# Optimization experiments

Measured on AMD Instinct MI355X. Metric: run time of the kernel, lower is better.

Reference implementation:

```python
import jax, jax.numpy as jnp
import numpy as np

# Dims (see shape_source)
B, C_IN, H, W = 32, 256, 56, 56
O, J = 256, 64            # out_channels, in_connects (sparse in-channel subset per out channel)
KH, KW = 3, 3
STRIDE = (1, 1)
PAD = (1, 1)


def setup_inputs() -> dict:
    key = jax.random.key(0)
    k1, k2 = jax.random.split(key)
    x = jax.random.normal(k1, (B, C_IN, H, W), dtype=jnp.float32)
    # init_rand_indices: each out channel samples in_connects distinct in-channels
    rng = np.random.default_rng(0)
    w_idx = jnp.asarray(
        np.stack([rng.permutation(C_IN)[:J] for _ in range(O)]), dtype=jnp.int32
    )  # [O, J]
    # reset_parameters: uniform(-stdv, +stdv), stdv = 1/sqrt(in_connects * kh * kw)
    stdv = 1.0 / np.sqrt(J * KH * KW)
    w_vals = jax.random.uniform(k2, (O, J, KH, KW), dtype=jnp.float32,
                                minval=-stdv, maxval=stdv)
    return {"x": x, "w_vals": w_vals, "w_idx": w_idx}


def reference(x, w_vals, w_idx):
    # Sparse conv: out[b,o] = sum_j conv(x[:, w_idx[o,j]], w_vals[o,j]).
    # Equivalent math: scatter sparse weights into a dense [O, C_in, KH, KW]
    # kernel (zeros on unselected channels) and run one dense conv.
    dense_w = jnp.zeros((O, C_IN, KH, KW), dtype=w_vals.dtype)
    dense_w = dense_w.at[jnp.arange(O)[:, None], w_idx].set(w_vals)
    out = jax.lax.conv_general_dilated(
        x, dense_w,
        window_strides=STRIDE,
        padding=[(PAD[0], PAD[0]), (PAD[1], PAD[1])],
        dimension_numbers=("NCHW", "OIHW", "NCHW"),
    )  # [B, O, H, W]
    return out
```

## Files before the change

### kernel.cpp

```cpp
#include <hip/hip_runtime.h>
#include <hip/hip_bf16.h>


typedef __attribute__((ext_vector_type(8))) short bf16x8;
typedef __attribute__((ext_vector_type(4))) float f32x4;

#define WD_BYTES 1179648
#define XP_BYTES 55115776
#define WS_NEED  (WD_BYTES + XP_BYTES)
#define ABUF  32768
#define BHOFF 65536
#define LDS_TOT (65536 + 49152)

__global__ __launch_bounds__(256) void preproc(
    const float* __restrict__ x, const float* __restrict__ wv,
    const int* __restrict__ widx, __hip_bfloat16* __restrict__ wd,
    __hip_bfloat16* __restrict__ xp)
{
    int bid = blockIdx.x;
    int tid = threadIdx.x;
    if (bid >= 1792) {
        int o = bid - 1792;
        int j = tid & 63;
        if (tid < 64) {
#pragma unroll
            for (int k = 0; k < 9; ++k)
                reinterpret_cast<float2*>(wd + (size_t)k * 65536 + o * 256)[j] =
                    float2{0.f, 0.f};
        }
        __syncthreads();
        if (tid < 64) {
            int cin = widx[o * 64 + j];
            const float* src = wv + (size_t)(o * 64 + j) * 9;
#pragma unroll
            for (int k = 0; k < 9; ++k)
                wd[(size_t)k * 65536 + o * 256 + cin] = __float2bfloat16(src[k]);
        }
        return;
    }
    int b = bid / 56, h = bid - (bid / 56) * 56;
    __shared__ __hip_bfloat16 tile[56][264];
    int c = tid;
    const float* src = x + ((size_t)(b * 256 + c)) * 3136 + h * 56;
    float vals[56];
#pragma unroll
    for (int i = 0; i < 14; ++i) {
        float4 v = *reinterpret_cast<const float4*>(src + i * 4);
        vals[i*4+0] = v.x; vals[i*4+1] = v.y; vals[i*4+2] = v.z; vals[i*4+3] = v.w;
    }
#pragma unroll
    for (int w = 0; w < 56; ++w) tile[w][c] = __float2bfloat16(vals[w]);

    char* rowb = (char*)xp + (((size_t)b * 58 + (h + 1)) * 58) * 512;
    if (tid < 64)        reinterpret_cast<double*>(rowb)[tid] = 0.0;
    else if (tid < 128)  *reinterpret_cast<double*>(rowb + 57 * 512 + (tid - 64) * 8) = 0.0;
    if (h == 0) {
        char* r0 = (char*)xp + (((size_t)b * 58 + 0) * 58) * 512;
        for (int i = tid; i < 58 * 64; i += 256) reinterpret_cast<double*>(r0)[i] = 0.0;
    }
    if (h == 55) {
        char* r57 = (char*)xp + (((size_t)b * 58 + 57) * 58) * 512;
        for (int i = tid; i < 58 * 64; i += 256) reinterpret_cast<double*>(r57)[i] = 0.0;
    }

    __syncthreads();
    char* obase = (char*)xp + (((size_t)b * 58 + (h + 1)) * 58) * 512;
#pragma unroll
    for (int k = 0; k < 7; ++k) {
        int i = tid + k * 256;
        int w = i >> 5, cc = i & 31;
        bf16x8 v = *reinterpret_cast<const bf16x8*>(&tile[w][cc * 8]);
        *reinterpret_cast<bf16x8*>(obase + (size_t)(w + 1) * 512 + cc * 16) = v;
    }
}


__device__ __forceinline__ void gload_lds16(const void* g, void* l) {
    __builtin_amdgcn_global_load_lds(
        (const __attribute__((address_space(1))) void*)g,
        (__attribute__((address_space(3))) void*)l, 16, 0, 0);
}

__device__ __forceinline__ void stage_a4(const char* wdB, char* smem, int dstA,
                                         int wid, int sa_off, int aoff) {
#pragma unroll
    for (int J = 0; J < 4; ++J)
        gload_lds16(wdB + aoff + J * 32768 + sa_off,
                    smem + dstA + (J * 64 + wid * 8) * 128);
}

__device__ __forceinline__ void stage_bh6(const char* xpOcs, char* smem, int wid,
                                          const int (&srcp)[6]) {
#pragma unroll
    for (int j = 0; j < 6; ++j)
        gload_lds16(xpOcs + srcp[j], smem + BHOFF + j * 8192 + wid * 1024);
}

#define BAR() __builtin_amdgcn_s_barrier()
#define VMCNT0() asm volatile("s_waitcnt vmcnt(0)" ::: "memory")

__global__ __launch_bounds__(512, 2) void sparse_conv_mfma224(
    const __hip_bfloat16* __restrict__ wd, const __hip_bfloat16* __restrict__ xp,
    float* __restrict__ out)
{
    extern __shared__ char smem[];
    const char* wdB = (const char*)wd;
    const char* xpB = (const char*)xp;

    const int bid = blockIdx.x;
    const int nt = (bid & 7) * 56 + (bid >> 3);

    const int t = threadIdx.x;
    const int lane = t & 63, wid = t >> 6;
    const int wr = wid >> 1, wc = wid & 1;

    const int axor = (((lane & 7) ^ (lane >> 3)) * 16);
    const int sa_off = (wid * 8 + (lane >> 3)) * 512 + axor;

    const int a_rb = (lane & 15) * 128;
    const int xq0 = (((lane >> 4)) ^ (lane & 7)) * 16;
    const int xq1 = ((4 + (lane >> 4)) ^ (lane & 7)) * 16;
    const int wrOff = wr * 8192;

    const int p0 = nt * 224;
    const int bImg = p0 / 3136;
    const int r0 = (p0 - bImg * 3136) / 56;
    const char* xpO = xpB + (size_t)((bImg * 58 + r0) * 58) * 512;

    int srcp[6];
#pragma unroll
    for (int j = 0; j < 6; ++j) {
        int beta = j * 8192 + wid * 1024 + lane * 16;
        int rb = beta >> 7;
        int c  = (beta >> 4) & 7;
        srcp[j] = (rb < 348) ? (rb * 512 + ((c ^ (rb & 7)) << 4)) : 0;
    }

    int rowpl[7];
#pragma unroll
    for (int n = 0; n < 7; ++n) {
        int q = wc * 112 + n * 16 + (lane & 15);
        int qr = q / 56;
        rowpl[n] = qr * 58 + (q - qr * 56);
    }
    const int g4 = lane >> 4;

    f32x4 acc[4][7] = {};

    stage_bh6(xpO, smem, wid, srcp);
    stage_a4(wdB, smem, 0, wid, sa_off, 0);
    VMCNT0();
    BAR();

    int k9 = 0, cs = 0, shift = 0;
    for (int g = 0; g < 36; ++g) {
        int k9n = k9 + 1, csn = cs;
        if (k9n == 9) { k9n = 0; csn = cs + 1; if (csn == 4) csn = 0; }
        stage_a4(wdB, smem, ((g + 1) & 1) * ABUF, wid, sa_off,
                 k9n * 131072 + csn * 128);

        const int abase = (g & 1) * ABUF + wrOff + a_rb;
        bf16x8 af0[4], af1[4], bf0[7], bf1[7];
#pragma unroll
        for (int mi = 0; mi < 4; ++mi) {
            af0[mi] = *(const bf16x8*)(smem + abase + mi * 2048 + xq0);
            af1[mi] = *(const bf16x8*)(smem + abase + mi * 2048 + xq1);
        }
#pragma unroll
        for (int n = 0; n < 7; ++n) {
            int roff = rowpl[n] + shift;
            int ba = BHOFF + (roff << 7) + ((g4 ^ (roff & 7)) << 4);
            bf0[n] = *(const bf16x8*)(smem + ba);
            bf1[n] = *(const bf16x8*)(smem + (ba ^ 64));
        }

        __builtin_amdgcn_s_setprio(1);
#pragma unroll
        for (int mi = 0; mi < 4; ++mi)
#pragma unroll
            for (int ni = 0; ni < 7; ++ni)
                acc[mi][ni] = __builtin_amdgcn_mfma_f32_16x16x32_bf16(
                    af0[mi], bf0[ni], acc[mi][ni], 0, 0, 0);
#pragma unroll
        for (int mi = 0; mi < 4; ++mi)
#pragma unroll
            for (int ni = 0; ni < 7; ++ni)
                acc[mi][ni] = __builtin_amdgcn_mfma_f32_16x16x32_bf16(
                    af1[mi], bf1[ni], acc[mi][ni], 0, 0, 0);
        __builtin_amdgcn_s_setprio(0);

        VMCNT0();
        BAR();

        if (k9n == 0) {
            if (csn != 0) {
                stage_bh6(xpO + csn * 128, smem, wid, srcp);
                VMCNT0();
                BAR();
            }
            shift = 0;
        } else {
            shift += ((k9n % 3) == 0) ? 56 : 1;
        }
        k9 = k9n; cs = csn;
    }

#pragma unroll
    for (int n = 0; n < 7; ++n) {
        int p = nt * 224 + wc * 112 + n * 16;
        int pb = p / 3136;
        int rem0 = p - pb * 3136;
#pragma unroll
        for (int m = 0; m < 4; ++m) {
            int o = wr * 64 + m * 16 + (lane >> 4) * 4;
            float* dst = out + ((size_t)(pb * 256 + o)) * 3136 + rem0 + (lane & 15);
#pragma unroll
            for (int r = 0; r < 4; ++r) dst[(size_t)r * 3136] = acc[m][n][r];
        }
    }
}


__global__ __launch_bounds__(256) void sparse_conv_direct(
    const float* __restrict__ x, const float* __restrict__ wv,
    const int* __restrict__ widx, float* __restrict__ out)
{
    const int bid = blockIdx.x;
    const int b = bid >> 8, o = bid & 255;
    const int tid = threadIdx.x;
    __shared__ float plane[58 * 60];
    const int rt = tid >> 3, ct = tid & 7;
    const int r0 = rt * 2, c0 = ct * 7;
    const bool active = (rt < 28);
    float acc[2][7];
#pragma unroll
    for (int i = 0; i < 2; ++i)
#pragma unroll
        for (int c = 0; c < 7; ++c) acc[i][c] = 0.f;
    const float* xb = x + (size_t)b * 256 * 3136;
    const int* idxp = widx + o * 64;
    const float* wp0 = wv + (size_t)o * 64 * 9;
    for (int j = 0; j < 64; ++j) {
        const int cin = idxp[j];
        const float* src = xb + cin * 3136;
        __syncthreads();
        for (int i = tid; i < 58 * 58; i += 256) {
            const int r = i / 58, c = i - r * 58;
            const int h = r - 1, w = c - 1;
            float v = 0.f;
            if ((unsigned)h < 56u && (unsigned)w < 56u) v = src[h * 56 + w];
            plane[r * 60 + c] = v;
        }
        float wreg[9];
#pragma unroll
        for (int k = 0; k < 9; ++k) wreg[k] = wp0[j * 9 + k];
        __syncthreads();
        if (active) {
            float rows[4][9];
#pragma unroll
            for (int dr = 0; dr < 4; ++dr)
#pragma unroll
                for (int cc = 0; cc < 9; ++cc)
                    rows[dr][cc] = plane[(r0 + dr) * 60 + (c0 + cc)];
#pragma unroll
            for (int i = 0; i < 2; ++i)
#pragma unroll
                for (int cc = 0; cc < 7; ++cc) {
                    float s = acc[i][cc];
#pragma unroll
                    for (int kh = 0; kh < 3; ++kh)
#pragma unroll
                        for (int kw = 0; kw < 3; ++kw)
                            s += rows[i + kh][cc + kw] * wreg[kh * 3 + kw];
                    acc[i][cc] = s;
                }
        }
    }
    if (active) {
        float* op = out + (size_t)bid * 3136;
#pragma unroll
        for (int i = 0; i < 2; ++i)
#pragma unroll
            for (int cc = 0; cc < 7; ++cc)
                op[(r0 + i) * 56 + (c0 + cc)] = acc[i][cc];
    }
}

extern "C" void kernel_launch(void* const* d_in, const int* in_sizes, int n_in,
                              void* d_out, int out_size, void* d_ws, size_t ws_size,
                              hipStream_t stream) {
    const float* x    = (const float*)d_in[0];
    const float* wv   = (const float*)d_in[1];
    const int*   widx = (const int*)d_in[2];
    float* out = (float*)d_out;
    (void)in_sizes; (void)n_in; (void)out_size;

    if (ws_size < (size_t)WS_NEED) {
        sparse_conv_direct<<<dim3(32 * 256), dim3(256), 0, stream>>>(x, wv, widx, out);
        return;
    }

    __hip_bfloat16* wd = (__hip_bfloat16*)d_ws;
    __hip_bfloat16* xp = (__hip_bfloat16*)((char*)d_ws + WD_BYTES);

    preproc<<<dim3(32 * 56 + 256), dim3(256), 0, stream>>>(x, wv, widx, wd, xp);

    (void)hipFuncSetAttribute((const void*)sparse_conv_mfma224,
                              hipFuncAttributeMaxDynamicSharedMemorySize, LDS_TOT);
    sparse_conv_mfma224<<<dim3(448), dim3(512), LDS_TOT, stream>>>(wd, xp, out);
}
```

Baseline: 150.0 us.

## Triple-buffer weight tiles and split K-halves to overlap LDS reads with MFMA

```diff
diff --git a/kernel.cpp b/kernel.cpp
--- a/kernel.cpp
+++ b/kernel.cpp
@@ -9,8 +9,8 @@
 #define XP_BYTES 55115776
 #define WS_NEED  (WD_BYTES + XP_BYTES)
 #define ABUF  32768
-#define BHOFF 65536
-#define LDS_TOT (65536 + 49152)
+#define BHOFF 98304
+#define LDS_TOT 147456
 
 __global__ __launch_bounds__(256) void preproc(
     const float* __restrict__ x, const float* __restrict__ wv,
@@ -99,6 +99,67 @@
 #define BAR() __builtin_amdgcn_s_barrier()
 #define VMCNT0() asm volatile("s_waitcnt vmcnt(0)" ::: "memory")
 
+__device__ __forceinline__ void mfma28(bf16x8 (&af)[4], bf16x8 (&bf)[7],
+                                       f32x4 (&acc)[4][7]) {
+    __builtin_amdgcn_s_setprio(1);
+#pragma unroll
+    for (int mi = 0; mi < 4; ++mi)
+#pragma unroll
+        for (int ni = 0; ni < 7; ++ni)
+            acc[mi][ni] = __builtin_amdgcn_mfma_f32_16x16x32_bf16(
+                af[mi], bf[ni], acc[mi][ni], 0, 0, 0);
+    __builtin_amdgcn_s_setprio(0);
+}
+
+template<int TJ>
+__device__ __forceinline__ void iter_normal(
+    const char* wdB, char* smem, int cs,
+    int wid, int sa_off, int wrOff, int a_rb, int xq0, int xq1, int g4,
+    const int (&rowpl)[7], bf16x8 (&bf0)[7], f32x4 (&acc)[4][7])
+{
+    constexpr int E   = TJ % 3;
+    constexpr int E2  = (TJ + 2) % 3;
+    constexpr int SH  = (TJ / 3) * 58 + (TJ % 3);
+    constexpr int SHN = ((TJ + 1) / 3) * 58 + ((TJ + 1) % 3);
+
+    bf16x8 af1[4], bf1[7];
+    {
+        const int abase = E * ABUF + wrOff + a_rb;
+#pragma unroll
+        for (int mi = 0; mi < 4; ++mi)
+            af1[mi] = *(const bf16x8*)(smem + abase + mi * 2048 + xq1);
+#pragma unroll
+        for (int n = 0; n < 7; ++n) {
+            int roff = rowpl[n] + SH;
+            int ba = BHOFF + (roff << 7) + (((g4 ^ (roff & 7)) << 4) ^ 64);
+            bf1[n] = *(const bf16x8*)(smem + ba);
+        }
+    }
+    VMCNT0();
+    BAR();
+    bf16x8 af0[4];
+    {
+        const int abase = E * ABUF + wrOff + a_rb;
+#pragma unroll
+        for (int mi = 0; mi < 4; ++mi)
+            af0[mi] = *(const bf16x8*)(smem + abase + mi * 2048 + xq0);
+    }
+    mfma28(af0, bf0, acc);
+    {
+        int aoff2;
+        if constexpr (TJ <= 6) aoff2 = (TJ + 2) * 131072 + cs * 128;
+        else                   aoff2 = ((cs + 1) & 3) * 128;
+        stage_a4(wdB, smem, E2 * ABUF, wid, sa_off, aoff2);
+    }
+#pragma unroll
+    for (int n = 0; n < 7; ++n) {
+        int roff = rowpl[n] + SHN;
+        int ba = BHOFF + (roff << 7) + ((g4 ^ (roff & 7)) << 4);
+        bf0[n] = *(const bf16x8*)(smem + ba);
+    }
+    mfma28(af1, bf1, acc);
+}
+
 __global__ __launch_bounds__(512, 2) void sparse_conv_mfma224(
     const __hip_bfloat16* __restrict__ wd, const __hip_bfloat16* __restrict__ xp,
     float* __restrict__ out)
@@ -146,63 +207,64 @@
     const int g4 = lane >> 4;
 
     f32x4 acc[4][7] = {};
+    bf16x8 bf0[7];
 
     stage_bh6(xpO, smem, wid, srcp);
     stage_a4(wdB, smem, 0, wid, sa_off, 0);
     VMCNT0();
     BAR();
-
-    int k9 = 0, cs = 0, shift = 0;
-    for (int g = 0; g < 36; ++g) {
-        int k9n = k9 + 1, csn = cs;
-        if (k9n == 9) { k9n = 0; csn = cs + 1; if (csn == 4) csn = 0; }
-        stage_a4(wdB, smem, ((g + 1) & 1) * ABUF, wid, sa_off,
-                 k9n * 131072 + csn * 128);
-
-        const int abase = (g & 1) * ABUF + wrOff + a_rb;
-        bf16x8 af0[4], af1[4], bf0[7], bf1[7];
-#pragma unroll
-        for (int mi = 0; mi < 4; ++mi) {
-            af0[mi] = *(const bf16x8*)(smem + abase + mi * 2048 + xq0);
-            af1[mi] = *(const bf16x8*)(smem + abase + mi * 2048 + xq1);
-        }
-#pragma unroll
-        for (int n = 0; n < 7; ++n) {
-            int roff = rowpl[n] + shift;
-            int ba = BHOFF + (roff << 7) + ((g4 ^ (roff & 7)) << 4);
-            bf0[n] = *(const bf16x8*)(smem + ba);
-            bf1[n] = *(const bf16x8*)(smem + (ba ^ 64));
-        }
-
-        __builtin_amdgcn_s_setprio(1);
-#pragma unroll
-        for (int mi = 0; mi < 4; ++mi)
-#pragma unroll
-            for (int ni = 0; ni < 7; ++ni)
-                acc[mi][ni] = __builtin_amdgcn_mfma_f32_16x16x32_bf16(
-                    af0[mi], bf0[ni], acc[mi][ni], 0, 0, 0);
-#pragma unroll
-        for (int mi = 0; mi < 4; ++mi)
-#pragma unroll
-            for (int ni = 0; ni < 7; ++ni)
-                acc[mi][ni] = __builtin_amdgcn_mfma_f32_16x16x32_bf16(
-                    af1[mi], bf1[ni], acc[mi][ni], 0, 0, 0);
-        __builtin_amdgcn_s_setprio(0);
-
-        VMCNT0();
-        BAR();
-
-        if (k9n == 0) {
-            if (csn != 0) {
-                stage_bh6(xpO + csn * 128, smem, wid, srcp);
+#pragma unroll
+    for (int n = 0; n < 7; ++n) {
+        int roff = rowpl[n];
+        int ba = BHOFF + (roff << 7) + ((g4 ^ (roff & 7)) << 4);
+        bf0[n] = *(const bf16x8*)(smem + ba);
+    }
+    stage_a4(wdB, smem, ABUF, wid, sa_off, 131072);
+
+    for (int cs = 0; cs < 4; ++cs) {
+        iter_normal<0>(wdB, smem, cs, wid, sa_off, wrOff, a_rb, xq0, xq1, g4, rowpl, bf0, acc);
+        iter_normal<1>(wdB, smem, cs, wid, sa_off, wrOff, a_rb, xq0, xq1, g4, rowpl, bf0, acc);
+        iter_normal<2>(wdB, smem, cs, wid, sa_off, wrOff, a_rb, xq0, xq1, g4, rowpl, bf0, acc);
+        iter_normal<3>(wdB, smem, cs, wid, sa_off, wrOff, a_rb, xq0, xq1, g4, rowpl, bf0, acc);
+        iter_normal<4>(wdB, smem, cs, wid, sa_off, wrOff, a_rb, xq0, xq1, g4, rowpl, bf0, acc);
+        iter_normal<5>(wdB, smem, cs, wid, sa_off, wrOff, a_rb, xq0, xq1, g4, rowpl, bf0, acc);
+        iter_normal<6>(wdB, smem, cs, wid, sa_off, wrOff, a_rb, xq0, xq1, g4, rowpl, bf0, acc);
+        iter_normal<7>(wdB, smem, cs, wid, sa_off, wrOff, a_rb, xq0, xq1, g4, rowpl, bf0, acc);
+
+        {
+            bf16x8 af1[4], bf1[7], af0[4];
+            const int abase = 2 * ABUF + wrOff + a_rb;
+#pragma unroll
+            for (int mi = 0; mi < 4; ++mi)
+                af1[mi] = *(const bf16x8*)(smem + abase + mi * 2048 + xq1);
+#pragma unroll
+            for (int n = 0; n < 7; ++n) {
+                int roff = rowpl[n] + 118;
+                int ba = BHOFF + (roff << 7) + (((g4 ^ (roff & 7)) << 4) ^ 64);
+                bf1[n] = *(const bf16x8*)(smem + ba);
+            }
+            VMCNT0();
+            BAR();
+#pragma unroll
+            for (int mi = 0; mi < 4; ++mi)
+                af0[mi] = *(const bf16x8*)(smem + abase + mi * 2048 + xq0);
+            mfma28(af0, bf0, acc);
+            mfma28(af1, bf1, acc);
+
+            if (cs < 3) {
+                BAR();
+                stage_bh6(xpO + (cs + 1) * 128, smem, wid, srcp);
+                stage_a4(wdB, smem, ABUF, wid, sa_off, 131072 + (cs + 1) * 128);
                 VMCNT0();
                 BAR();
+#pragma unroll
+                for (int n = 0; n < 7; ++n) {
+                    int roff = rowpl[n];
+                    int ba = BHOFF + (roff << 7) + ((g4 ^ (roff & 7)) << 4);
+                    bf0[n] = *(const bf16x8*)(smem + ba);
+                }
             }
-            shift = 0;
-        } else {
-            shift += ((k9n % 3) == 0) ? 56 : 1;
-        }
-        k9 = k9n; cs = csn;
+        }
     }
 
 #pragma unroll
```

New measurement: 416.4 us. 2.78x slower.

## Split output channels across two blocks to halve tile size and double grid

Applied to the files above, without the earlier changes.

```diff
diff --git a/kernel.cpp b/kernel.cpp
--- a/kernel.cpp
+++ b/kernel.cpp
@@ -8,9 +8,9 @@
 #define WD_BYTES 1179648
 #define XP_BYTES 55115776
 #define WS_NEED  (WD_BYTES + XP_BYTES)
-#define ABUF  32768
-#define BHOFF 65536
-#define LDS_TOT (65536 + 49152)
+#define ABUF  16384
+#define BHOFF 32768
+#define LDS_TOT 77824
 
 __global__ __launch_bounds__(256) void preproc(
     const float* __restrict__ x, const float* __restrict__ wv,
@@ -85,21 +85,26 @@
                                          int wid, int sa_off, int aoff) {
 #pragma unroll
     for (int J = 0; J < 4; ++J)
-        gload_lds16(wdB + aoff + J * 32768 + sa_off,
-                    smem + dstA + (J * 64 + wid * 8) * 128);
-}
-
-__device__ __forceinline__ void stage_bh6(const char* xpOcs, char* smem, int wid,
-                                          const int (&srcp)[6]) {
-#pragma unroll
-    for (int j = 0; j < 6; ++j)
-        gload_lds16(xpOcs + srcp[j], smem + BHOFF + j * 8192 + wid * 1024);
+        gload_lds16(wdB + aoff + J * 16384 + sa_off,
+                    smem + dstA + (J * 32 + wid * 8) * 128);
+}
+
+__device__ __forceinline__ void stage_bh11(const char* xpOcs, char* smem,
+                                           int wid, int lane) {
+#pragma unroll
+    for (int j = 0; j < 11; ++j) {
+        int beta = j * 4096 + wid * 1024 + lane * 16;
+        int rb = beta >> 7;
+        int c  = (beta >> 4) & 7;
+        int src = (rb < 348) ? (rb * 512 + ((c ^ (rb & 7)) << 4)) : 0;
+        gload_lds16(xpOcs + src, smem + BHOFF + j * 4096 + wid * 1024);
+    }
 }
 
 #define BAR() __builtin_amdgcn_s_barrier()
 #define VMCNT0() asm volatile("s_waitcnt vmcnt(0)" ::: "memory")
 
-__global__ __launch_bounds__(512, 2) void sparse_conv_mfma224(
+__global__ __launch_bounds__(256, 2) void sparse_conv_mfma2b(
     const __hip_bfloat16* __restrict__ wd, const __hip_bfloat16* __restrict__ xp,
     float* __restrict__ out)
 {
@@ -108,7 +113,9 @@
     const char* xpB = (const char*)xp;
 
     const int bid = blockIdx.x;
-    const int nt = (bid & 7) * 56 + (bid >> 3);
+    const int swz = (bid & 7) * 112 + (bid >> 3);
+    const int mt = swz & 1;
+    const int nt = swz >> 1;
 
     const int t = threadIdx.x;
     const int lane = t & 63, wid = t >> 6;
@@ -116,6 +123,7 @@
 
     const int axor = (((lane & 7) ^ (lane >> 3)) * 16);
     const int sa_off = (wid * 8 + (lane >> 3)) * 512 + axor;
+    const int mtOff = mt * 65536;
 
     const int a_rb = (lane & 15) * 128;
     const int xq0 = (((lane >> 4)) ^ (lane & 7)) * 16;
@@ -127,15 +135,6 @@
     const int r0 = (p0 - bImg * 3136) / 56;
     const char* xpO = xpB + (size_t)((bImg * 58 + r0) * 58) * 512;
 
-    int srcp[6];
-#pragma unroll
-    for (int j = 0; j < 6; ++j) {
-        int beta = j * 8192 + wid * 1024 + lane * 16;
-        int rb = beta >> 7;
-        int c  = (beta >> 4) & 7;
-        srcp[j] = (rb < 348) ? (rb * 512 + ((c ^ (rb & 7)) << 4)) : 0;
-    }
-
     int rowpl[7];
 #pragma unroll
     for (int n = 0; n < 7; ++n) {
@@ -147,8 +146,8 @@
 
     f32x4 acc[4][7] = {};
 
-    stage_bh6(xpO, smem, wid, srcp);
-    stage_a4(wdB, smem, 0, wid, sa_off, 0);
+    stage_bh11(xpO, smem, wid, lane);
+    stage_a4(wdB, smem, 0, wid, sa_off, mtOff);
     VMCNT0();
     BAR();
 
@@ -157,7 +156,7 @@
         int k9n = k9 + 1, csn = cs;
         if (k9n == 9) { k9n = 0; csn = cs + 1; if (csn == 4) csn = 0; }
         stage_a4(wdB, smem, ((g + 1) & 1) * ABUF, wid, sa_off,
-                 k9n * 131072 + csn * 128);
+                 k9n * 131072 + mtOff + csn * 128);
 
         const int abase = (g & 1) * ABUF + wrOff + a_rb;
         bf16x8 af0[4], af1[4], bf0[7], bf1[7];
@@ -194,7 +193,7 @@
 
         if (k9n == 0) {
             if (csn != 0) {
-                stage_bh6(xpO + csn * 128, smem, wid, srcp);
+                stage_bh11(xpO + csn * 128, smem, wid, lane);
                 VMCNT0();
                 BAR();
             }
@@ -212,7 +211,7 @@
         int rem0 = p - pb * 3136;
 #pragma unroll
         for (int m = 0; m < 4; ++m) {
-            int o = wr * 64 + m * 16 + (lane >> 4) * 4;
+            int o = mt * 128 + wr * 64 + m * 16 + (lane >> 4) * 4;
             float* dst = out + ((size_t)(pb * 256 + o)) * 3136 + rem0 + (lane & 15);
 #pragma unroll
             for (int r = 0; r < 4; ++r) dst[(size_t)r * 3136] = acc[m][n][r];
@@ -305,7 +304,7 @@
 
     preproc<<<dim3(32 * 56 + 256), dim3(256), 0, stream>>>(x, wv, widx, wd, xp);
 
-    (void)hipFuncSetAttribute((const void*)sparse_conv_mfma224,
+    (void)hipFuncSetAttribute((const void*)sparse_conv_mfma2b,
                               hipFuncAttributeMaxDynamicSharedMemorySize, LDS_TOT);
-    sparse_conv_mfma224<<<dim3(448), dim3(512), LDS_TOT, stream>>>(wd, xp, out);
-}
+    sparse_conv_mfma2b<<<dim3(896), dim3(256), LDS_TOT, stream>>>(wd, xp, out);
+}
```

Measured after the change: 125.4 us, median of 3. 1.2x faster.
